# Kernel tuning notes

Measured on AMD Instinct MI355X. Metric: run time of the kernel, lower is better.

## Reference

```python
import jax, jax.numpy as jnp
import numpy as np

B, C, H, W = 2, 64, 256, 256
P = 3          # n_pyramids
NO = 16        # per-pyramid output channels
FEX = P * NO   # 48
N = 32768      # |yi| = mask.sum()


def _conv(x, w):
    return jax.lax.conv_general_dilated(
        x, w, window_strides=(1, 1), padding='SAME',
        dimension_numbers=('NCHW', 'OIHW', 'NCHW'))


def _mask_weight(mask):
    # MaskedConv: w = mask / clamp(avg3x3(mask), 1e-8)  (computed under no_grad)
    avg = jnp.ones((1, 1, 3, 3), mask.dtype) / 9.0
    wm = _conv(mask, avg)
    return jax.lax.stop_gradient(mask / jnp.clip(wm, 1e-8))


def _mconv(x, w, wm):
    return _conv(x, w) * wm


def _resblock(x, w1, w2, mask, wm):
    x = mask * x
    r = jax.nn.relu(_mconv(x, w1, wm))
    r = _mconv(r, w2, wm)
    return x + r


def setup_inputs() -> dict:
    key = jax.random.key(0)
    ks = jax.random.split(key, 12)
    rng = np.random.default_rng(0)
    yi_np = np.sort(rng.choice(H * W, size=N, replace=False)).astype(np.int32)
    mask_flat = np.zeros(H * W, np.float32)
    mask_flat[yi_np] = 1.0
    mask = jnp.asarray(mask_flat).reshape(1, 1, H, W)
    # near-identity homography (3x3)
    m = jnp.asarray(np.array([[0.9, 0.05, 2.0],
                              [-0.03, 1.1, -1.0],
                              [1e-4, -2e-4, 1.0]], np.float32))
    s = 0.05
    return {
        'xs': jax.random.normal(ks[0], (P, B, C, H, W), jnp.float32),
        'mask': mask,
        'yi': jnp.asarray(yi_np),
        'm': m,
        'ss_res_w': s * jax.random.normal(ks[1], (P, 2, 2, C, C, 3, 3), jnp.float32),
        'ss_out_w': s * jax.random.normal(ks[2], (P, NO, C, 3, 3), jnp.float32),
        'feat_res_w': s * jax.random.normal(ks[3], (2, 2, FEX, FEX, 3, 3), jnp.float32),
        'samp_w1': s * jax.random.normal(ks[4], (FEX, FEX + 1), jnp.float32),
        'samp_b1': s * jax.random.normal(ks[5], (FEX,), jnp.float32),
        'samp_w2': s * jax.random.normal(ks[6], (FEX, FEX), jnp.float32),
        'samp_b2': s * jax.random.normal(ks[7], (FEX,), jnp.float32),
        'samp_w3': s * jax.random.normal(ks[8], (P, FEX), jnp.float32),
        'samp_b3': s * jax.random.normal(ks[9], (P,), jnp.float32),
    }


def reference(xs, mask, yi, m, ss_res_w, ss_out_w, feat_res_w,
              samp_w1, samp_b1, samp_w2, samp_b2, samp_w3, samp_b3):
    wm = _mask_weight(mask)
    # ---- MSResFeature: per-pyramid MaskedResSeq(64->64->16, depth=3) ----
    feats = []
    for i in range(P):  # small fixed loop over pyramids
        x = mask * xs[i]
        x = _resblock(x, ss_res_w[i, 0, 0], ss_res_w[i, 0, 1], mask, wm)
        x = _resblock(x, ss_res_w[i, 1, 0], ss_res_w[i, 1, 1], mask, wm)
        x = _mconv(x, ss_out_w[i], wm)
        feats.append(x)
    f = jnp.concatenate(feats, axis=1)  # (B, 48, H, W)
    # shared trunk: MaskedResSeq(48->48->48, depth=3), residual
    g = mask * f
    g = _resblock(g, feat_res_w[0, 0], feat_res_w[0, 1], mask, wm)
    g = _resblock(g, feat_res_w[1, 0], feat_res_w[1, 1], mask, wm)
    f = f + g
    b = f.shape[0]
    # ---- gather at sparse indices yi ----
    ff = f.reshape(b, FEX, -1)[:, :, yi]  # (B, 48, N)
    # ---- dsda: |Jacobian det| of projective warp, log-scaled (no_grad) ----
    ygrid, xgrid = jnp.meshgrid(jnp.arange(H, dtype=f.dtype),
                                jnp.arange(W, dtype=f.dtype), indexing='ij')
    wcoord = m[2, 0] * xgrid + m[2, 1] * ygrid + m[2, 2]
    dsda = jnp.abs(jnp.linalg.det(m)) / jnp.clip(jnp.abs(wcoord), 1e-8) ** 3
    dsda = jnp.log(dsda.reshape(-1)[yi] + 1e-8)
    dsda = jax.lax.stop_gradient(jnp.broadcast_to(dsda[None, None, :], (b, 1, N)))
    h = jnp.concatenate((ff, dsda), axis=1)  # (B, 49, N)
    # ---- 1x1 Conv1d sampler MLP ----
    h = jax.nn.relu(jnp.einsum('oc,bcn->bon', samp_w1, h) + samp_b1[None, :, None])
    h = jax.nn.relu(jnp.einsum('oc,bcn->bon', samp_w2, h) + samp_b2[None, :, None])
    p = jnp.einsum('oc,bcn->bon', samp_w3, h) + samp_b3[None, :, None]  # (B, 3, N)
    # ---- scatter back to dense grid and blend pyramids ----
    ws = jnp.zeros((b, P, H * W), f.dtype).at[:, :, yi].set(p)
    ws = ws.reshape(b, P, H, W)
    out = jnp.sum(ws.transpose(1, 0, 2, 3)[:, :, None] * xs, axis=0)  # (B, C, H, W)
    return out
```

## Files before the change

### kernel.cpp

```cpp
#include <hip/hip_runtime.h>
#include <hip/hip_bf16.h>

typedef unsigned short ushort_t;
typedef __attribute__((ext_vector_type(8))) short short8;
typedef __attribute__((ext_vector_type(4))) short short4v;
typedef __attribute__((ext_vector_type(4))) float f32x4;

constexpr int Hh = 256, Ww = 256, HW = Hh * Ww;
constexpr int Bb = 2, Cc = 64, Pp = 3, NOo = 16, FEXc = 48, Nn = 32768;
constexpr int TW = 32, TH = 4;
constexpr int HALOP = (TH + 2) * 34;
constexpr int AROWS = 208;
constexpr int PADH = 72;

__device__ inline ushort_t f2bf(float v) {
    __hip_bfloat16 h = __float2bfloat16(v);
    return *(ushort_t*)&h;
}
__device__ inline float bf2f(ushort_t u) {
    __hip_bfloat16 h = *(__hip_bfloat16*)&u;
    return __bfloat162float(h);
}
__device__ inline void gload_lds16(const ushort_t* g, ushort_t* l) {
    __builtin_amdgcn_global_load_lds(
        (const __attribute__((address_space(1))) unsigned int*)g,
        (__attribute__((address_space(3))) unsigned int*)l, 16, 0, 0);
}

__global__ __launch_bounds__(256) void k_wm(const float* __restrict__ mask,
                                            float* __restrict__ wm,
                                            float* __restrict__ zpage) {
    int pos = blockIdx.x * 256 + threadIdx.x;
    if (blockIdx.x == 0 && threadIdx.x < 64) zpage[threadIdx.x] = 0.f;
    int h = pos >> 8, w = pos & 255;
    float s = 0.f;
    #pragma unroll
    for (int dy = -1; dy <= 1; ++dy)
        #pragma unroll
        for (int dx = -1; dx <= 1; ++dx) {
            int hh = h + dy, ww = w + dx;
            if (hh >= 0 && hh < Hh && ww >= 0 && ww < Ww) s += mask[hh * Ww + ww];
        }
    float avg = s * (1.f / 9.f);
    wm[pos] = mask[pos] / fmaxf(avg, 1e-8f);
}

__global__ __launch_bounds__(256) void k_zero(float4* __restrict__ p) {
    p[blockIdx.x * 256 + threadIdx.x] = make_float4(0.f, 0.f, 0.f, 0.f);
}

__global__ __launch_bounds__(256) void k_wx_res(const float* __restrict__ src,
                                                ushort_t* __restrict__ dst) {
    int idx = blockIdx.x * 256 + threadIdx.x;
    int j = idx / 36864; int rem = idx - j * 36864;
    int t = rem >> 12; int o = (rem >> 6) & 63; int c = rem & 63;
    dst[idx] = f2bf(src[j * 36864 + o * 576 + c * 9 + t]);
}
__global__ __launch_bounds__(256) void k_wx_out(const float* __restrict__ src,
                                                ushort_t* __restrict__ dst) {
    int idx = blockIdx.x * 256 + threadIdx.x;
    int i = idx / 9216; int rem = idx - i * 9216;
    int t = rem >> 10; int o = (rem >> 6) & 15; int c = rem & 63;
    dst[idx] = f2bf(src[i * 9216 + o * 576 + c * 9 + t]);
}
__global__ __launch_bounds__(256) void k_wx_trunk(const float* __restrict__ src,
                                                  ushort_t* __restrict__ dst) {
    int idx = blockIdx.x * 256 + threadIdx.x;
    int j = idx / 27648; int rem = idx - j * 27648;
    int t = rem / 3072; int rem2 = rem - t * 3072;
    int o = rem2 >> 6; int c = rem2 & 63;
    float v = (c < 48) ? src[j * (48 * 48 * 9) + o * 432 + c * 9 + t] : 0.f;
    dst[idx] = f2bf(v);
}
__global__ __launch_bounds__(256) void k_wx_mlp(
    const float* __restrict__ w1, const float* __restrict__ b1,
    const float* __restrict__ w2, const float* __restrict__ b2,
    const float* __restrict__ w3, const float* __restrict__ b3,
    ushort_t* __restrict__ dst) {
    int idx = blockIdx.x * 256 + threadIdx.x;
    float v = 0.f;
    if (idx < 3072) {
        int o = idx >> 6, c = idx & 63;
        v = (c < 49) ? w1[o * 49 + c] : (c == 49 ? b1[o] : 0.f);
    } else if (idx < 6144) {
        int o = (idx - 3072) >> 6, c = idx & 63;
        v = (c < 48) ? w2[o * 48 + c] : (c == 48 ? b2[o] : 0.f);
    } else {
        int o = (idx - 6144) >> 6, c = idx & 63;
        if (o < 3) v = (c < 48) ? w3[o * 48 + c] : (c == 49 ? b3[o] : 0.f);
    }
    dst[idx] = f2bf(v);
}

__global__ __launch_bounds__(256) void k_xm(const float* __restrict__ xs,
                                            const float* __restrict__ mask,
                                            ushort_t* __restrict__ X) {
    __shared__ float l[64 * 65];
    const int p0 = blockIdx.x * 64;
    const size_t zoff = (size_t)blockIdx.y * 64 * HW;
    const int tid = threadIdx.x;
    const int px = tid & 63;
    const float mv = mask[p0 + px];
    #pragma unroll
    for (int k = 0; k < 16; ++k) {
        int c = (tid >> 6) + 4 * k;
        l[c * 65 + px] = xs[zoff + (size_t)c * HW + p0 + px] * mv;
    }
    __syncthreads();
    #pragma unroll
    for (int k = 0; k < 2; ++k) {
        int idx = tid + k * 256;
        int p = idx >> 3, c8 = idx & 7;
        short8 v;
        #pragma unroll
        for (int i = 0; i < 8; ++i) v[i] = (short)f2bf(l[(c8 * 8 + i) * 65 + p]);
        *(short8*)&X[zoff + (size_t)(p0 + p) * 64 + c8 * 8] = v;
    }
}

template <int OC, int MODE, bool TOF>
__global__ __launch_bounds__(256) void k_mconv(
    const ushort_t* __restrict__ in,
    const ushort_t* __restrict__ wgt, int wstride,
    const float* __restrict__ wm,
    const ushort_t* __restrict__ zp,
    const ushort_t* __restrict__ base,
    ushort_t* __restrict__ out) {
    constexpr int NM = OC / 16;
    constexpr int WROWS = 9 * OC;
    constexpr int WDMA = WROWS / 16;
    __shared__ __align__(1024) ushort_t alds[AROWS * 64];
    __shared__ __align__(1024) ushort_t wlds[WROWS * 32];
    const int tid = threadIdx.x;
    const int wv = tid >> 6;
    const int ln = tid & 63;
    const int w0 = blockIdx.x * TW, h0 = blockIdx.y * TH;
    const int zz = blockIdx.z;
    const ushort_t* inb = in + (size_t)zz * HW * 64;
    const ushort_t* wB = wgt + (size_t)(zz >> 1) * wstride;
    const ushort_t* baseb = base ? base + (size_t)zz * HW * 64 : nullptr;
    ushort_t* outb = TOF ? out + (size_t)(zz & 1) * HW * 64 : out + (size_t)zz * HW * 64;
    const int ocb = TOF ? (zz >> 1) * 16 : 0;

    const int lo = ln & 15, slr = ln >> 4, g8 = slr * 8;

    f32x4 acc[NM][2];
    #pragma unroll
    for (int mf = 0; mf < NM; ++mf)
        #pragma unroll
        for (int nf = 0; nf < 2; ++nf) acc[mf][nf] = (f32x4){0.f, 0.f, 0.f, 0.f};

    #pragma unroll
    for (int k = 0; k < 7; ++k) {
        int s = wv + 4 * k;
        if (s < 26) {
            int pp = s * 8 + (ln >> 3);
            int r = (pp * 241) >> 13;
            int col = pp - r * 34;
            int gh = h0 + r - 1, gw = w0 + col - 1;
            bool ok = (pp < HALOP) & (gh >= 0) & (gh < Hh) & (gw >= 0) & (gw < Ww);
            int che = ((ln & 7) ^ (pp & 7)) << 3;
            const ushort_t* src = ok ? inb + (size_t)(gh * Ww + gw) * 64 + che : zp + che;
            gload_lds16(src, &alds[s * 512]);
        }
    }

    #pragma unroll
    for (int h = 0; h < 2; ++h) {
        if (h) __syncthreads();
        #pragma unroll
        for (int k = 0; k < (WDMA + 3) / 4; ++k) {
            int s = wv + 4 * k;
            if (s < WDMA) {
                int r = s * 16 + (ln >> 2);
                int d = ln & 3;
                int j = d ^ ((r ^ (r >> 2)) & 3);
                gload_lds16(wB + (size_t)r * 64 + h * 32 + j * 8, &wlds[s * 512]);
            }
        }
        asm volatile("s_waitcnt vmcnt(0)" ::: "memory");
        __syncthreads();

        #pragma unroll
        for (int dy = 0; dy < 3; ++dy)
            #pragma unroll
            for (int dx = 0; dx < 3; ++dx) {
                const int t = dy * 3 + dx;
                short8 bfr[2];
                #pragma unroll
                for (int nf = 0; nf < 2; ++nf) {
                    int pp2 = (wv + dy) * 34 + nf * 16 + lo + dx;
                    bfr[nf] = *(const short8*)
                        &alds[pp2 * 64 + (((h * 4 + slr) ^ (pp2 & 7)) << 3)];
                }
                short8 afr[NM];
                #pragma unroll
                for (int mf = 0; mf < NM; ++mf) {
                    int r = t * OC + mf * 16 + lo;
                    afr[mf] = *(const short8*)
                        &wlds[r * 32 + ((slr ^ ((r ^ (r >> 2)) & 3)) << 3)];
                }
                #pragma unroll
                for (int mf = 0; mf < NM; ++mf)
                    #pragma unroll
                    for (int nf = 0; nf < 2; ++nf)
                        acc[mf][nf] = __builtin_amdgcn_mfma_f32_16x16x32_bf16(
                            afr[mf], bfr[nf], acc[mf][nf], 0, 0, 0);
            }
    }

    #pragma unroll
    for (int nf = 0; nf < 2; ++nf) {
        int r = h0 + wv;
        int x = w0 + nf * 16 + lo;
        int pos = r * Ww + x;
        float wmv = wm[pos];
        #pragma unroll
        for (int mf = 0; mf < NM; ++mf) {
            int o0 = ocb + mf * 16 + slr * 4;
            size_t oi = (size_t)pos * 64 + o0;
            float v[4];
            #pragma unroll
            for (int j = 0; j < 4; ++j) v[j] = acc[mf][nf][j] * wmv;
            if (MODE == 0) {
                #pragma unroll
                for (int j = 0; j < 4; ++j) v[j] = fmaxf(v[j], 0.f);
            } else if (MODE == 1) {
                short4v bv = *(const short4v*)&baseb[oi];
                #pragma unroll
                for (int j = 0; j < 4; ++j) v[j] += bf2f((ushort_t)bv[j]);
            }
            short4v sv;
            #pragma unroll
            for (int j = 0; j < 4; ++j) sv[j] = (short)f2bf(v[j]);
            *(short4v*)&outb[oi] = sv;
        }
    }
}

__global__ __launch_bounds__(256) void k_gather_mlp(
    const ushort_t* __restrict__ F, const ushort_t* __restrict__ G,
    const int* __restrict__ yi, const float* __restrict__ m,
    const ushort_t* __restrict__ wA1, const ushort_t* __restrict__ wA2,
    const ushort_t* __restrict__ wA3, float* __restrict__ pvd) {
    __shared__ __align__(16) ushort_t HA[4 * 16 * PADH];
    __shared__ __align__(16) ushort_t HB[4 * 16 * PADH];
    const int tid = threadIdx.x, wv = tid >> 6, ln = tid & 63;
    ushort_t* ha = HA + wv * 16 * PADH;
    ushort_t* hb = HB + wv * 16 * PADH;
    const int t0 = blockIdx.x * 64 + wv * 16;
    const int b = t0 >> 15;
    const int lo = ln & 15, g8 = (ln >> 4) * 8;

    #pragma unroll
    for (int rnd = 0; rnd < 2; ++rnd) {
        int j = rnd * 64 + ln;
        if (j < 96) {
            int pt = j / 6, sl = j - pt * 6;
            int n = (t0 + pt) & (Nn - 1);
            int pos = yi[n];
            size_t gi = ((size_t)(b * HW) + pos) * 64 + sl * 8;
            short8 fa = *(const short8*)&F[gi];
            short8 ga = *(const short8*)&G[gi];
            short8 sv;
            #pragma unroll
            for (int i = 0; i < 8; ++i)
                sv[i] = (short)f2bf(bf2f((ushort_t)fa[i]) + bf2f((ushort_t)ga[i]));
            *(short8*)&ha[pt * PADH + sl * 8] = sv;
        }
    }
    if (ln < 16) {
        int pt = ln;
        int n = (t0 + pt) & (Nn - 1);
        int pos = yi[n];
        float det = m[0] * (m[4] * m[8] - m[5] * m[7])
                  - m[1] * (m[3] * m[8] - m[5] * m[6])
                  + m[2] * (m[3] * m[7] - m[4] * m[6]);
        int yr = pos >> 8, xc = pos & 255;
        float wc = m[6] * (float)xc + m[7] * (float)yr + m[8];
        float cw = fmaxf(fabsf(wc), 1e-8f);
        float dsda = fabsf(det) / (cw * cw * cw);
        float ld = logf(dsda + 1e-8f);
        const ushort_t one = f2bf(1.0f);
        short8 z = {0, 0, 0, 0, 0, 0, 0, 0};
        short8 sa = z; sa[0] = (short)f2bf(ld); sa[1] = (short)one;
        short8 sb = z; sb[0] = (short)one;
        *(short8*)&ha[pt * PADH + 48] = sa;
        *(short8*)&ha[pt * PADH + 56] = z;
        *(short8*)&hb[pt * PADH + 48] = sb;
        *(short8*)&hb[pt * PADH + 56] = z;
    }
    asm volatile("s_waitcnt lgkmcnt(0)" ::: "memory");

    f32x4 a1[3] = {{0.f,0.f,0.f,0.f},{0.f,0.f,0.f,0.f},{0.f,0.f,0.f,0.f}};
    #pragma unroll
    for (int ks = 0; ks < 2; ++ks) {
        short8 bf = *(const short8*)&ha[lo * PADH + ks * 32 + g8];
        #pragma unroll
        for (int mf = 0; mf < 3; ++mf) {
            short8 af = *(const short8*)&wA1[(mf * 16 + lo) * 64 + ks * 32 + g8];
            a1[mf] = __builtin_amdgcn_mfma_f32_16x16x32_bf16(af, bf, a1[mf], 0, 0, 0);
        }
    }
    #pragma unroll
    for (int mf = 0; mf < 3; ++mf) {
        short4v sv;
        #pragma unroll
        for (int j = 0; j < 4; ++j) sv[j] = (short)f2bf(fmaxf(a1[mf][j], 0.f));
        *(short4v*)&hb[lo * PADH + mf * 16 + (ln >> 4) * 4] = sv;
    }
    asm volatile("s_waitcnt lgkmcnt(0)" ::: "memory");

    f32x4 a2[3] = {{0.f,0.f,0.f,0.f},{0.f,0.f,0.f,0.f},{0.f,0.f,0.f,0.f}};
    #pragma unroll
    for (int ks = 0; ks < 2; ++ks) {
        short8 bf = *(const short8*)&hb[lo * PADH + ks * 32 + g8];
        #pragma unroll
        for (int mf = 0; mf < 3; ++mf) {
            short8 af = *(const short8*)&wA2[(mf * 16 + lo) * 64 + ks * 32 + g8];
            a2[mf] = __builtin_amdgcn_mfma_f32_16x16x32_bf16(af, bf, a2[mf], 0, 0, 0);
        }
    }
    #pragma unroll
    for (int mf = 0; mf < 3; ++mf) {
        short4v sv;
        #pragma unroll
        for (int j = 0; j < 4; ++j) sv[j] = (short)f2bf(fmaxf(a2[mf][j], 0.f));
        *(short4v*)&ha[lo * PADH + mf * 16 + (ln >> 4) * 4] = sv;
    }
    asm volatile("s_waitcnt lgkmcnt(0)" ::: "memory");

    f32x4 a3 = {0.f, 0.f, 0.f, 0.f};
    #pragma unroll
    for (int ks = 0; ks < 2; ++ks) {
        short8 bf = *(const short8*)&ha[lo * PADH + ks * 32 + g8];
        short8 af = *(const short8*)&wA3[lo * 64 + ks * 32 + g8];
        a3 = __builtin_amdgcn_mfma_f32_16x16x32_bf16(af, bf, a3, 0, 0, 0);
    }
    if (ln < 16) {
        int n = (t0 + lo) & (Nn - 1);
        int pos = yi[n];
        #pragma unroll
        for (int j = 0; j < 3; ++j)
            pvd[(size_t)(b * Pp + j) * HW + pos] = a3[j];
    }
}

__global__ __launch_bounds__(256) void k_blend(const float4* __restrict__ xs,
                                               const float4* __restrict__ pvd,
                                               float4* __restrict__ out) {
    int i = blockIdx.x * 256 + threadIdx.x;
    int pos4 = i & (HW / 4 - 1);
    int bc = i >> 14;
    int b = bc >> 6;
    float4 acc = make_float4(0.f, 0.f, 0.f, 0.f);
    #pragma unroll
    for (int p = 0; p < Pp; ++p) {
        float4 pv = pvd[(b * Pp + p) * (HW / 4) + pos4];
        float4 x = xs[p * (Bb * Cc * HW / 4) + i];
        acc.x += pv.x * x.x;
        acc.y += pv.y * x.y;
        acc.z += pv.z * x.z;
        acc.w += pv.w * x.w;
    }
    out[i] = acc;
}

extern "C" void kernel_launch(void* const* d_in, const int* in_sizes, int n_in,
                              void* d_out, int out_size, void* d_ws, size_t ws_size,
                              hipStream_t stream) {
    const float* xs        = (const float*)d_in[0];
    const float* mask      = (const float*)d_in[1];
    const int*   yi        = (const int*)d_in[2];
    const float* m         = (const float*)d_in[3];
    const float* ss_res_w  = (const float*)d_in[4];
    const float* ss_out_w  = (const float*)d_in[5];
    const float* feat_res_w= (const float*)d_in[6];
    const float* w1 = (const float*)d_in[7];
    const float* b1 = (const float*)d_in[8];
    const float* w2 = (const float*)d_in[9];
    const float* b2 = (const float*)d_in[10];
    const float* w3 = (const float*)d_in[11];
    const float* b3 = (const float*)d_in[12];

    float* wm    = (float*)d_ws;
    float* zpage = wm + HW;
    float* pvd   = zpage + 64;
    ushort_t* wB = (ushort_t*)(pvd + (size_t)Bb * Pp * HW);
    constexpr size_t RES_T = 12 * 9 * 64 * 64;
    constexpr size_t OUT_T = 3 * 9 * 16 * 64;
    constexpr size_t TRK_T = 4 * 9 * 48 * 64;
    constexpr size_t MLP_T = 7168;
    constexpr size_t ZT = (size_t)Pp * Bb * HW * 64;
    ushort_t* wA = wB + RES_T + OUT_T + TRK_T;
    ushort_t* X = wA + MLP_T;
    ushort_t* U = X + ZT;
    ushort_t* V = U + ZT;
    ushort_t* F = V + ZT;
    ushort_t* G = F + (size_t)Bb * HW * 64;
    const ushort_t* zp = (const ushort_t*)zpage;

    k_wm<<<HW / 256, 256, 0, stream>>>(mask, wm, zpage);
    k_wx_res  <<<RES_T / 256, 256, 0, stream>>>(ss_res_w, wB);
    k_wx_out  <<<OUT_T / 256, 256, 0, stream>>>(ss_out_w, wB + RES_T);
    k_wx_trunk<<<TRK_T / 256, 256, 0, stream>>>(feat_res_w, wB + RES_T + OUT_T);
    k_wx_mlp  <<<MLP_T / 256, 256, 0, stream>>>(w1, b1, w2, b2, w3, b3, wA);

    const dim3 gridP(Ww / TW, Hh / TH, Pp * Bb);
    const dim3 gridT(Ww / TW, Hh / TH, Bb);
    const int RS = 4 * 9 * 64 * 64;
    const int OS = 9 * 16 * 64;

    k_xm<<<dim3(HW / 64, Pp * Bb), 256, 0, stream>>>(xs, mask, X);
    k_mconv<64, 0, false><<<gridP, 256, 0, stream>>>(X, wB,             RS, wm, zp, nullptr, U);
    k_mconv<64, 1, false><<<gridP, 256, 0, stream>>>(U, wB + 1 * 36864, RS, wm, zp, X,       V);
    k_mconv<64, 0, false><<<gridP, 256, 0, stream>>>(V, wB + 2 * 36864, RS, wm, zp, nullptr, U);
    k_mconv<64, 1, false><<<gridP, 256, 0, stream>>>(U, wB + 3 * 36864, RS, wm, zp, V,       V);
    k_mconv<16, 2, true ><<<gridP, 256, 0, stream>>>(V, wB + RES_T,     OS, wm, zp, nullptr, F);

    const ushort_t* tw = wB + RES_T + OUT_T;
    k_mconv<48, 0, false><<<gridT, 256, 0, stream>>>(F, tw,             0, wm, zp, nullptr, U);
    k_mconv<48, 1, false><<<gridT, 256, 0, stream>>>(U, tw + 1 * 27648, 0, wm, zp, F,       G);
    k_mconv<48, 0, false><<<gridT, 256, 0, stream>>>(G, tw + 2 * 27648, 0, wm, zp, nullptr, U);
    k_mconv<48, 1, false><<<gridT, 256, 0, stream>>>(U, tw + 3 * 27648, 0, wm, zp, G,       G);

    k_zero<<<(Bb * Pp * HW / 4) / 256, 256, 0, stream>>>((float4*)pvd);
    k_gather_mlp<<<Bb * Nn / 64, 256, 0, stream>>>(F, G, yi, m,
        wA, wA + 3072, wA + 6144, pvd);
    k_blend<<<(Bb * Cc * HW / 4) / 256, 256, 0, stream>>>((const float4*)xs, (const float4*)pvd,
                                                          (float4*)d_out);
}
```

Baseline: 329.8 us.

## Double conv tile height so each wave computes two output rows

Raises the masked-conv tile from 32x4 to 32x8 pixels, so each wave now covers two output rows with four N-fragments instead of two. The halo overhead per tile shrinks and each weight fragment loaded from LDS feeds twice as many MFMAs. Shared memory moves to a dynamically sized buffer, since the larger halo plus weights no longer fit the static layout. The cost is more accumulator registers and more LDS per block, which can lower occupancy, and half as many blocks, which may leave CUs idle on the smaller trunk grid.

```diff
diff --git a/kernel.cpp b/kernel.cpp
--- a/kernel.cpp
+++ b/kernel.cpp
@@ -8,9 +8,9 @@
 
 constexpr int Hh = 256, Ww = 256, HW = Hh * Ww;
 constexpr int Bb = 2, Cc = 64, Pp = 3, NOo = 16, FEXc = 48, Nn = 32768;
-constexpr int TW = 32, TH = 4;
+constexpr int TW = 32, TH = 8;
 constexpr int HALOP = (TH + 2) * 34;
-constexpr int AROWS = 208;
+constexpr int AROWS = 352;
 constexpr int PADH = 72;
 
 __device__ inline ushort_t f2bf(float v) {
@@ -129,8 +129,9 @@
     constexpr int NM = OC / 16;
     constexpr int WROWS = 9 * OC;
     constexpr int WDMA = WROWS / 16;
-    __shared__ __align__(1024) ushort_t alds[AROWS * 64];
-    __shared__ __align__(1024) ushort_t wlds[WROWS * 32];
+    extern __shared__ __align__(1024) ushort_t smem[];
+    ushort_t* alds = smem;
+    ushort_t* wlds = smem + AROWS * 64;
     const int tid = threadIdx.x;
     const int wv = tid >> 6;
     const int ln = tid & 63;
@@ -144,25 +145,23 @@
 
     const int lo = ln & 15, slr = ln >> 4, g8 = slr * 8;
 
-    f32x4 acc[NM][2];
+    f32x4 acc[NM][4];
     #pragma unroll
     for (int mf = 0; mf < NM; ++mf)
         #pragma unroll
-        for (int nf = 0; nf < 2; ++nf) acc[mf][nf] = (f32x4){0.f, 0.f, 0.f, 0.f};
-
-    #pragma unroll
-    for (int k = 0; k < 7; ++k) {
-        int s = wv + 4 * k;
-        if (s < 26) {
-            int pp = s * 8 + (ln >> 3);
-            int r = (pp * 241) >> 13;
-            int col = pp - r * 34;
-            int gh = h0 + r - 1, gw = w0 + col - 1;
-            bool ok = (pp < HALOP) & (gh >= 0) & (gh < Hh) & (gw >= 0) & (gw < Ww);
-            int che = ((ln & 7) ^ (pp & 7)) << 3;
-            const ushort_t* src = ok ? inb + (size_t)(gh * Ww + gw) * 64 + che : zp + che;
-            gload_lds16(src, &alds[s * 512]);
-        }
+        for (int nf = 0; nf < 4; ++nf) acc[mf][nf] = (f32x4){0.f, 0.f, 0.f, 0.f};
+
+    #pragma unroll
+    for (int k = 0; k < 11; ++k) {
+        int s = wv * 11 + k;
+        int pp = s * 8 + (ln >> 3);
+        int r = (pp * 241) >> 13;
+        int col = pp - r * 34;
+        int gh = h0 + r - 1, gw = w0 + col - 1;
+        bool ok = (pp < HALOP) & (gh >= 0) & (gh < Hh) & (gw >= 0) & (gw < Ww);
+        int che = ((ln & 7) ^ (pp & 7)) << 3;
+        const ushort_t* src = ok ? inb + (size_t)(gh * Ww + gw) * 64 + che : zp + che;
+        gload_lds16(src, &alds[s * 512]);
     }
 
     #pragma unroll
@@ -186,10 +185,10 @@
             #pragma unroll
             for (int dx = 0; dx < 3; ++dx) {
                 const int t = dy * 3 + dx;
-                short8 bfr[2];
+                short8 bfr[4];
                 #pragma unroll
-                for (int nf = 0; nf < 2; ++nf) {
-                    int pp2 = (wv + dy) * 34 + nf * 16 + lo + dx;
+                for (int nf = 0; nf < 4; ++nf) {
+                    int pp2 = (2 * wv + (nf >> 1) + dy) * 34 + (nf & 1) * 16 + lo + dx;
                     bfr[nf] = *(const short8*)
                         &alds[pp2 * 64 + (((h * 4 + slr) ^ (pp2 & 7)) << 3)];
                 }
@@ -203,16 +202,16 @@
                 #pragma unroll
                 for (int mf = 0; mf < NM; ++mf)
                     #pragma unroll
-                    for (int nf = 0; nf < 2; ++nf)
+                    for (int nf = 0; nf < 4; ++nf)
                         acc[mf][nf] = __builtin_amdgcn_mfma_f32_16x16x32_bf16(
                             afr[mf], bfr[nf], acc[mf][nf], 0, 0, 0);
             }
     }
 
     #pragma unroll
-    for (int nf = 0; nf < 2; ++nf) {
-        int r = h0 + wv;
-        int x = w0 + nf * 16 + lo;
+    for (int nf = 0; nf < 4; ++nf) {
+        int r = h0 + 2 * wv + (nf >> 1);
+        int x = w0 + (nf & 1) * 16 + lo;
         int pos = r * Ww + x;
         float wmv = wm[pos];
         #pragma unroll
@@ -410,19 +409,22 @@
     const dim3 gridT(Ww / TW, Hh / TH, Bb);
     const int RS = 4 * 9 * 64 * 64;
     const int OS = 9 * 16 * 64;
+    constexpr size_t SH64 = (size_t)AROWS * 128 + 9 * 64 * 64;
+    constexpr size_t SH48 = (size_t)AROWS * 128 + 9 * 48 * 64;
+    constexpr size_t SH16 = (size_t)AROWS * 128 + 9 * 16 * 64;
 
     k_xm<<<dim3(HW / 64, Pp * Bb), 256, 0, stream>>>(xs, mask, X);
-    k_mconv<64, 0, false><<<gridP, 256, 0, stream>>>(X, wB,             RS, wm, zp, nullptr, U);
-    k_mconv<64, 1, false><<<gridP, 256, 0, stream>>>(U, wB + 1 * 36864, RS, wm, zp, X,       V);
-    k_mconv<64, 0, false><<<gridP, 256, 0, stream>>>(V, wB + 2 * 36864, RS, wm, zp, nullptr, U);
-    k_mconv<64, 1, false><<<gridP, 256, 0, stream>>>(U, wB + 3 * 36864, RS, wm, zp, V,       V);
-    k_mconv<16, 2, true ><<<gridP, 256, 0, stream>>>(V, wB + RES_T,     OS, wm, zp, nullptr, F);
+    k_mconv<64, 0, false><<<gridP, 256, SH64, stream>>>(X, wB,             RS, wm, zp, nullptr, U);
+    k_mconv<64, 1, false><<<gridP, 256, SH64, stream>>>(U, wB + 1 * 36864, RS, wm, zp, X,       V);
+    k_mconv<64, 0, false><<<gridP, 256, SH64, stream>>>(V, wB + 2 * 36864, RS, wm, zp, nullptr, U);
+    k_mconv<64, 1, false><<<gridP, 256, SH64, stream>>>(U, wB + 3 * 36864, RS, wm, zp, V,       V);
+    k_mconv<16, 2, true ><<<gridP, 256, SH16, stream>>>(V, wB + RES_T,     OS, wm, zp, nullptr, F);
 
     const ushort_t* tw = wB + RES_T + OUT_T;
-    k_mconv<48, 0, false><<<gridT, 256, 0, stream>>>(F, tw,             0, wm, zp, nullptr, U);
-    k_mconv<48, 1, false><<<gridT, 256, 0, stream>>>(U, tw + 1 * 27648, 0, wm, zp, F,       G);
-    k_mconv<48, 0, false><<<gridT, 256, 0, stream>>>(G, tw + 2 * 27648, 0, wm, zp, nullptr, U);
-    k_mconv<48, 1, false><<<gridT, 256, 0, stream>>>(U, tw + 3 * 27648, 0, wm, zp, G,       G);
+    k_mconv<48, 0, false><<<gridT, 256, SH48, stream>>>(F, tw,             0, wm, zp, nullptr, U);
+    k_mconv<48, 1, false><<<gridT, 256, SH48, stream>>>(U, tw + 1 * 27648, 0, wm, zp, F,       G);
+    k_mconv<48, 0, false><<<gridT, 256, SH48, stream>>>(G, tw + 2 * 27648, 0, wm, zp, nullptr, U);
+    k_mconv<48, 1, false><<<gridT, 256, SH48, stream>>>(U, tw + 3 * 27648, 0, wm, zp, G,       G);
 
     k_zero<<<(Bb * Pp * HW / 4) / 256, 256, 0, stream>>>((float4*)pvd);
     k_gather_mlp<<<Bb * Nn / 64, 256, 0, stream>>>(F, G, yi, m,
```

After: 324.5 us. Within noise of the previous version (-1.6%).

## Split masked-conv weights into output-channel groups with double-buffered LDS staging

Applied to the files above, without the earlier changes.

The conv kernel now processes output channels in groups of 32, staging each group's weight half (K-half) into one of two LDS buffers while the other is consumed, using partial vmcnt waits to overlap weight loads with MFMA work. This shrinks the weight LDS footprint (dynamic shared memory) and the accumulator register count, which may raise occupancy. The cost is more phases and barriers, and the activation halo is reread from LDS for each output group. The epilogue runs once per group after the second K-half.

```diff
diff --git a/kernel.cpp b/kernel.cpp
--- a/kernel.cpp
+++ b/kernel.cpp
@@ -9,8 +9,8 @@
 constexpr int Hh = 256, Ww = 256, HW = Hh * Ww;
 constexpr int Bb = 2, Cc = 64, Pp = 3, NOo = 16, FEXc = 48, Nn = 32768;
 constexpr int TW = 32, TH = 4;
-constexpr int HALOP = (TH + 2) * 34;
-constexpr int AROWS = 208;
+constexpr int HALOP4 = 6 * 34;
+constexpr int ASLOT = 26;
 constexpr int PADH = 72;
 
 __device__ inline ushort_t f2bf(float v) {
@@ -25,6 +25,12 @@
     __builtin_amdgcn_global_load_lds(
         (const __attribute__((address_space(1))) unsigned int*)g,
         (__attribute__((address_space(3))) unsigned int*)l, 16, 0, 0);
+}
+template <int N>
+__device__ __forceinline__ void wait_vm() {
+    if constexpr (N == 0) asm volatile("s_waitcnt vmcnt(0)" ::: "memory");
+    else if constexpr (N == 3) asm volatile("s_waitcnt vmcnt(3)" ::: "memory");
+    else if constexpr (N == 5) asm volatile("s_waitcnt vmcnt(5)" ::: "memory");
 }
 
 __global__ __launch_bounds__(256) void k_wm(const float* __restrict__ mask,
@@ -126,11 +132,14 @@
     const ushort_t* __restrict__ zp,
     const ushort_t* __restrict__ base,
     ushort_t* __restrict__ out) {
-    constexpr int NM = OC / 16;
-    constexpr int WROWS = 9 * OC;
-    constexpr int WDMA = WROWS / 16;
-    __shared__ __align__(1024) ushort_t alds[AROWS * 64];
-    __shared__ __align__(1024) ushort_t wlds[WROWS * 32];
+    constexpr int NG = (OC + 31) / 32;
+    constexpr int NPH = 2 * NG;
+    constexpr int WSLOT = (OC >= 48) ? 20 : 12;
+    constexpr int WV = WSLOT / 4;
+    extern __shared__ __align__(1024) ushort_t smem[];
+    ushort_t* alds  = smem;
+    ushort_t* wlds0 = smem + 208 * 64;
+    ushort_t* wlds1 = wlds0 + WSLOT * 512;
     const int tid = threadIdx.x;
     const int wv = tid >> 6;
     const int ln = tid & 63;
@@ -141,51 +150,80 @@
     const ushort_t* baseb = base ? base + (size_t)zz * HW * 64 : nullptr;
     ushort_t* outb = TOF ? out + (size_t)(zz & 1) * HW * 64 : out + (size_t)zz * HW * 64;
     const int ocb = TOF ? (zz >> 1) * 16 : 0;
-
-    const int lo = ln & 15, slr = ln >> 4, g8 = slr * 8;
-
-    f32x4 acc[NM][2];
-    #pragma unroll
-    for (int mf = 0; mf < NM; ++mf)
-        #pragma unroll
-        for (int nf = 0; nf < 2; ++nf) acc[mf][nf] = (f32x4){0.f, 0.f, 0.f, 0.f};
-
+    const int lo = ln & 15, slr = ln >> 4;
+
+    auto wstage = [&](int p, ushort_t* wbuf) {
+        const int gi = p >> 1, h = p & 1;
+        const int ob = gi * 32;
+        const int ocg = (OC - ob >= 32) ? 32 : 16;
+        #pragma unroll
+        for (int k = 0; k < WV; ++k) {
+            int s = wv + 4 * k;
+            int rl = s * 16 + (ln >> 2);
+            int d = ln & 3;
+            int j = d ^ ((rl ^ (rl >> 2)) & 3);
+            int t, ol;
+            if (ocg == 32) { t = rl >> 5; ol = rl & 31; }
+            else           { t = rl >> 4; ol = rl & 15; }
+            bool valid = rl < 9 * ocg;
+            const ushort_t* src = valid
+                ? wB + (size_t)(t * OC + ob + ol) * 64 + h * 32 + j * 8
+                : wB + j * 8;
+            gload_lds16(src, &wbuf[s * 512]);
+        }
+    };
+
+    wstage(0, wlds0);
     #pragma unroll
     for (int k = 0; k < 7; ++k) {
         int s = wv + 4 * k;
-        if (s < 26) {
+        if (s < ASLOT) {
             int pp = s * 8 + (ln >> 3);
             int r = (pp * 241) >> 13;
             int col = pp - r * 34;
             int gh = h0 + r - 1, gw = w0 + col - 1;
-            bool ok = (pp < HALOP) & (gh >= 0) & (gh < Hh) & (gw >= 0) & (gw < Ww);
+            bool ok = (pp < HALOP4) & (gh >= 0) & (gh < Hh) & (gw >= 0) & (gw < Ww);
             int che = ((ln & 7) ^ (pp & 7)) << 3;
             const ushort_t* src = ok ? inb + (size_t)(gh * Ww + gw) * 64 + che : zp + che;
             gload_lds16(src, &alds[s * 512]);
         }
     }
 
-    #pragma unroll
-    for (int h = 0; h < 2; ++h) {
-        if (h) __syncthreads();
-        #pragma unroll
-        for (int k = 0; k < (WDMA + 3) / 4; ++k) {
-            int s = wv + 4 * k;
-            if (s < WDMA) {
-                int r = s * 16 + (ln >> 2);
-                int d = ln & 3;
-                int j = d ^ ((r ^ (r >> 2)) & 3);
-                gload_lds16(wB + (size_t)r * 64 + h * 32 + j * 8, &wlds[s * 512]);
-            }
-        }
-        asm volatile("s_waitcnt vmcnt(0)" ::: "memory");
+    f32x4 acc[2][2];
+    #pragma unroll
+    for (int p = 0; p < NPH; ++p) {
+        const int gi = p >> 1, h = p & 1;
+        const int ob = gi * 32;
+        const int ocg = (OC - ob >= 32) ? 32 : 16;
+        const int nmg = ocg / 16;
+        ushort_t* wcur = (p & 1) ? wlds1 : wlds0;
+        if (p + 1 < NPH) {
+            wstage(p + 1, (p & 1) ? wlds0 : wlds1);
+            wait_vm<WV>();
+        } else {
+            wait_vm<0>();
+        }
         __syncthreads();
+
+        if (h == 0) {
+            #pragma unroll
+            for (int mfl = 0; mfl < 2; ++mfl)
+                #pragma unroll
+                for (int nf = 0; nf < 2; ++nf) acc[mfl][nf] = (f32x4){0.f, 0.f, 0.f, 0.f};
+        }
 
         #pragma unroll
         for (int dy = 0; dy < 3; ++dy)
             #pragma unroll
             for (int dx = 0; dx < 3; ++dx) {
                 const int t = dy * 3 + dx;
+                short8 afr[2];
+                #pragma unroll
+                for (int mfl = 0; mfl < 2; ++mfl) if (mfl < nmg) {
+                    int rl = t * ocg + mfl * 16 + lo;
+                    afr[mfl] = *(const short8*)
+                        &wcur[rl * 32 + ((slr ^ ((rl ^ (rl >> 2)) & 3)) << 3)];
+                }
                 short8 bfr[2];
                 #pragma unroll
                 for (int nf = 0; nf < 2; ++nf) {
@@ -193,48 +231,44 @@
                     bfr[nf] = *(const short8*)
                         &alds[pp2 * 64 + (((h * 4 + slr) ^ (pp2 & 7)) << 3)];
                 }
-                short8 afr[NM];
                 #pragma unroll
-                for (int mf = 0; mf < NM; ++mf) {
-                    int r = t * OC + mf * 16 + lo;
-                    afr[mf] = *(const short8*)
-                        &wlds[r * 32 + ((slr ^ ((r ^ (r >> 2)) & 3)) << 3)];
-                }
-                #pragma unroll
-                for (int mf = 0; mf < NM; ++mf)
+                for (int mfl = 0; mfl < 2; ++mfl) if (mfl < nmg)
                     #pragma unroll
                     for (int nf = 0; nf < 2; ++nf)
-                        acc[mf][nf] = __builtin_amdgcn_mfma_f32_16x16x32_bf16(
-                            afr[mf], bfr[nf], acc[mf][nf], 0, 0, 0);
+                        acc[mfl][nf] = __builtin_amdgcn_mfma_f32_16x16x32_bf16(
+                            afr[mfl], bfr[nf], acc[mfl][nf], 0, 0, 0);
             }
-    }
-
-    #pragma unroll
-    for (int nf = 0; nf < 2; ++nf) {
-        int r = h0 + wv;
-        int x = w0 + nf * 16 + lo;
-        int pos = r * Ww + x;
-        float wmv = wm[pos];
-        #pragma unroll
-        for (int mf = 0; mf < NM; ++mf) {
-            int o0 = ocb + mf * 16 + slr * 4;
-            size_t oi = (size_t)pos * 64 + o0;
-            float v[4];
+
+        if (h == 1) {
             #pragma unroll
-            for (int j = 0; j < 4; ++j) v[j] = acc[mf][nf][j] * wmv;
-            if (MODE == 0) {
+            for (int nf = 0; nf < 2; ++nf) {
+                int r = h0 + wv;
+                int x = w0 + nf * 16 + lo;
+                int pos = r * Ww + x;
+                float wmv = wm[pos];
                 #pragma unroll
-                for (int j = 0; j < 4; ++j) v[j] = fmaxf(v[j], 0.f);
-            } else if (MODE == 1) {
-                short4v bv = *(const short4v*)&baseb[oi];
-                #pragma unroll
-                for (int j = 0; j < 4; ++j) v[j] += bf2f((ushort_t)bv[j]);
+                for (int mfl = 0; mfl < 2; ++mfl) if (mfl < nmg) {
+                    int o0 = ocb + ob + mfl * 16 + slr * 4;
+                    size_t oi = (size_t)pos * 64 + o0;
+                    float v[4];
+                    #pragma unroll
+                    for (int q = 0; q < 4; ++q) v[q] = acc[mfl][nf][q] * wmv;
+                    if (MODE == 0) {
+                        #pragma unroll
+                        for (int q = 0; q < 4; ++q) v[q] = fmaxf(v[q], 0.f);
+                    } else if (MODE == 1) {
+                        short4v bv = *(const short4v*)&baseb[oi];
+                        #pragma unroll
+                        for (int q = 0; q < 4; ++q) v[q] += bf2f((ushort_t)bv[q]);
+                    }
+                    short4v sv;
+                    #pragma unroll
+                    for (int q = 0; q < 4; ++q) sv[q] = (short)f2bf(v[q]);
+                    *(short4v*)&outb[oi] = sv;
+                }
             }
-            short4v sv;
-            #pragma unroll
-            for (int j = 0; j < 4; ++j) sv[j] = (short)f2bf(v[j]);
-            *(short4v*)&outb[oi] = sv;
-        }
+        }
+        if (p + 1 < NPH) __syncthreads();
     }
 }
 
@@ -410,19 +444,22 @@
     const dim3 gridT(Ww / TW, Hh / TH, Bb);
     const int RS = 4 * 9 * 64 * 64;
     const int OS = 9 * 16 * 64;
+    constexpr size_t SH64 = 26624 + 2 * 20 * 1024;
+    constexpr size_t SH48 = SH64;
+    constexpr size_t SH16 = 26624 + 2 * 12 * 1024;
 
     k_xm<<<dim3(HW / 64, Pp * Bb), 256, 0, stream>>>(xs, mask, X);
-    k_mconv<64, 0, false><<<gridP, 256, 0, stream>>>(X, wB,             RS, wm, zp, nullptr, U);
-    k_mconv<64, 1, false><<<gridP, 256, 0, stream>>>(U, wB + 1 * 36864, RS, wm, zp, X,       V);
-    k_mconv<64, 0, false><<<gridP, 256, 0, stream>>>(V, wB + 2 * 36864, RS, wm, zp, nullptr, U);
-    k_mconv<64, 1, false><<<gridP, 256, 0, stream>>>(U, wB + 3 * 36864, RS, wm, zp, V,       V);
-    k_mconv<16, 2, true ><<<gridP, 256, 0, stream>>>(V, wB + RES_T,     OS, wm, zp, nullptr, F);
+    k_mconv<64, 0, false><<<gridP, 256, SH64, stream>>>(X, wB,             RS, wm, zp, nullptr, U);
+    k_mconv<64, 1, false><<<gridP, 256, SH64, stream>>>(U, wB + 1 * 36864, RS, wm, zp, X,       V);
+    k_mconv<64, 0, false><<<gridP, 256, SH64, stream>>>(V, wB + 2 * 36864, RS, wm, zp, nullptr, U);
+    k_mconv<64, 1, false><<<gridP, 256, SH64, stream>>>(U, wB + 3 * 36864, RS, wm, zp, V,       V);
+    k_mconv<16, 2, true ><<<gridP, 256, SH16, stream>>>(V, wB + RES_T,     OS, wm, zp, nullptr, F);
 
     const ushort_t* tw = wB + RES_T + OUT_T;
-    k_mconv<48, 0, false><<<gridT, 256, 0, stream>>>(F, tw,             0, wm, zp, nullptr, U);
-    k_mconv<48, 1, false><<<gridT, 256, 0, stream>>>(U, tw + 1 * 27648, 0, wm, zp, F,       G);
-    k_mconv<48, 0, false><<<gridT, 256, 0, stream>>>(G, tw + 2 * 27648, 0, wm, zp, nullptr, U);
-    k_mconv<48, 1, false><<<gridT, 256, 0, stream>>>(U, tw + 3 * 27648, 0, wm, zp, G,       G);
+    k_mconv<48, 0, false><<<gridT, 256, SH48, stream>>>(F, tw,             0, wm, zp, nullptr, U);
+    k_mconv<48, 1, false><<<gridT, 256, SH48, stream>>>(U, tw + 1 * 27648, 0, wm, zp, F,       G);
+    k_mconv<48, 0, false><<<gridT, 256, SH48, stream>>>(G, tw + 2 * 27648, 0, wm, zp, nullptr, U);
+    k_mconv<48, 1, false><<<gridT, 256, SH48, stream>>>(U, tw + 3 * 27648, 0, wm, zp, G,       G);
 
     k_zero<<<(Bb * Pp * HW / 4) / 256, 256, 0, stream>>>((float4*)pvd);
     k_gather_mlp<<<Bb * Nn / 64, 256, 0, stream>>>(F, G, yi, m,
```

Result: slower. 340.1 us (+3.1%).
